# Optimization experiments

Measured on AMD Instinct MI355X. Metric: run time of the kernel, lower is better.

The kernel has to match this reference:

```python
import jax, jax.numpy as jnp
import numpy as np

N_GROUPS = 8
TOPK_GROUPS = 4
TOPK = 8
ROUTE_SCALE = 2.5


def setup_inputs() -> dict:
    key = jax.random.key(0)
    k1, k2, k3 = jax.random.split(key, 3)
    T, D, E = 8192, 7168, 256
    x = jax.random.normal(k1, (T, D), dtype=jnp.float32)
    weight = jax.random.normal(k2, (E, D), dtype=jnp.float32) * 0.02
    bias = jax.random.normal(k3, (E,), dtype=jnp.float32) * 0.02
    return {"x": x, "weight": weight, "bias": bias}


def reference(x, weight, bias):
    T = x.shape[0]
    # gate linear + sigmoid scores (score_func == 'sigmoid', computed in fp32)
    logits = jnp.einsum("td,ed->te", x, weight)  # [T, E]
    scores = jax.nn.sigmoid(logits.astype(jnp.float32))
    origin_scores = scores
    s = scores + bias  # bias present since dim == 7168
    # grouped scores: [T, G, E/G]
    sg = s.reshape(T, N_GROUPS, -1)
    # bias branch: group score = sum of top-2 per group
    top2, _ = jax.lax.top_k(sg, 2)
    group_scores = top2.sum(axis=-1)  # [T, G]
    # keep top `topk_groups` groups, zero out the rest
    _, gidx = jax.lax.top_k(group_scores, TOPK_GROUPS)  # [T, topk_groups]
    mask = jax.nn.one_hot(gidx, N_GROUPS, dtype=sg.dtype).sum(axis=1)  # [T, G]
    s_masked = (sg * mask[:, :, None]).reshape(T, -1)  # [T, E]
    # per-token expert top-k on masked scores
    _, expert_indices = jax.lax.top_k(s_masked, TOPK)  # [T, topk]
    # gather unbiased scores, normalize (sigmoid branch), scale
    weights = jnp.take_along_axis(origin_scores, expert_indices, axis=-1)
    weights = weights / weights.sum(axis=-1, keepdims=True)
    weights = weights * ROUTE_SCALE
    return weights.astype(x.dtype), expert_indices
```

## Files before the change

kernel.cpp:

```cpp
#include <hip/hip_runtime.h>
#include <cmath>

#define TT 8192
#define NE 256
#define ND 7168
#define NGRP 8
#define TOPKG 4
#define TOPK 8
#define ROUTE_SCALE 2.5f

#define NKT (ND / 32)
#define NNT (NE / 16)

#define TM 64
#define XPITCH 40

typedef _Float16 half8_ __attribute__((ext_vector_type(8)));
typedef _Float16 half4_ __attribute__((ext_vector_type(4)));
typedef float float4_ __attribute__((ext_vector_type(4)));

__global__ __launch_bounds__(256) void conv_w_kernel(
    const float* __restrict__ w, _Float16* __restrict__ whF,
    _Float16* __restrict__ wlF)
{
    const int gid  = blockIdx.x * 256 + threadIdx.x;
    const int lane = gid & 63;
    const int pair = gid >> 6;
    const int kt   = pair % NKT;
    const int nt   = pair / NKT;
    const int n  = nt * 16 + (lane & 15);
    const int kb = kt * 32 + (lane >> 4) * 8;
    const float* src = w + (size_t)n * ND + kb;
    const float4 v0 = *reinterpret_cast<const float4*>(src);
    const float4 v1 = *reinterpret_cast<const float4*>(src + 4);
    const float vs[8] = {v0.x, v0.y, v0.z, v0.w, v1.x, v1.y, v1.z, v1.w};
    half8_ h, l;
    #pragma unroll
    for (int j = 0; j < 8; ++j) {
        const _Float16 hi = (_Float16)vs[j];
        h[j] = hi;
        l[j] = (_Float16)(vs[j] - (float)hi);
    }
    const size_t off = ((size_t)pair * 64 + lane) * 8;
    *reinterpret_cast<half8_*>(whF + off) = h;
    *reinterpret_cast<half8_*>(wlF + off) = l;
}

__global__ __launch_bounds__(256, 2) void gemm_kernel(
    const float* __restrict__ x, const _Float16* __restrict__ whF,
    const _Float16* __restrict__ wlF, float* __restrict__ partial,
    int K_slice)
{
    __shared__ _Float16 Xh[TM][XPITCH];
    __shared__ _Float16 Xl[TM][XPITCH];

    const int tid  = threadIdx.x;
    const int lane = tid & 63;
    const int nq   = tid >> 6;
    const int t0   = blockIdx.x * TM;
    const int ks   = blockIdx.y;
    const int kbeg = ks * K_slice;
    const int kt0  = kbeg >> 5;
    const int nchunks = K_slice >> 5;

    const int q  = lane >> 4;
    const int cn = lane & 15;

    float4_ acc[4][4];
    #pragma unroll
    for (int i = 0; i < 4; ++i)
        #pragma unroll
        for (int j = 0; j < 4; ++j) acc[i][j] = (float4_)0.0f;

    const int srow0 = tid >> 3;
    const int sc4   = tid & 7;

    for (int c = 0; c < nchunks; ++c) {
        const int k0 = kbeg + c * 32;
        #pragma unroll
        for (int i = 0; i < 2; ++i) {
            const int row = srow0 + i * 32;
            const float4 v = *reinterpret_cast<const float4*>(
                x + (size_t)(t0 + row) * ND + k0 + sc4 * 4);
            const float vs[4] = {v.x, v.y, v.z, v.w};
            half4_ h, l;
            #pragma unroll
            for (int j = 0; j < 4; ++j) {
                const _Float16 hi = (_Float16)vs[j];
                h[j] = hi;
                l[j] = (_Float16)(vs[j] - (float)hi);
            }
            *reinterpret_cast<half4_*>(&Xh[row][sc4 * 4]) = h;
            *reinterpret_cast<half4_*>(&Xl[row][sc4 * 4]) = l;
        }
        __syncthreads();

        half8_ ah[4], al[4];
        #pragma unroll
        for (int mt = 0; mt < 4; ++mt) {
            ah[mt] = *reinterpret_cast<const half8_*>(&Xh[mt * 16 + cn][q * 8]);
            al[mt] = *reinterpret_cast<const half8_*>(&Xl[mt * 16 + cn][q * 8]);
        }
        const int kt = kt0 + c;
        half8_ bh[4], bl[4];
        #pragma unroll
        for (int ntl = 0; ntl < 4; ++ntl) {
            const size_t off =
                ((size_t)((nq * 4 + ntl) * NKT + kt) * 64 + lane) * 8;
            bh[ntl] = *reinterpret_cast<const half8_*>(whF + off);
            bl[ntl] = *reinterpret_cast<const half8_*>(wlF + off);
        }
        #pragma unroll
        for (int mt = 0; mt < 4; ++mt)
            #pragma unroll
            for (int ntl = 0; ntl < 4; ++ntl) {
                acc[mt][ntl] = __builtin_amdgcn_mfma_f32_16x16x32_f16(
                    ah[mt], bh[ntl], acc[mt][ntl], 0, 0, 0);
                acc[mt][ntl] = __builtin_amdgcn_mfma_f32_16x16x32_f16(
                    al[mt], bh[ntl], acc[mt][ntl], 0, 0, 0);
                acc[mt][ntl] = __builtin_amdgcn_mfma_f32_16x16x32_f16(
                    ah[mt], bl[ntl], acc[mt][ntl], 0, 0, 0);
            }
        __syncthreads();
    }

    #pragma unroll
    for (int mt = 0; mt < 4; ++mt)
        #pragma unroll
        for (int r = 0; r < 4; ++r) {
            const int t = t0 + mt * 16 + q * 4 + r;
            float* rowp = partial + ((size_t)ks * TT + t) * NE;
            #pragma unroll
            for (int ntl = 0; ntl < 4; ++ntl)
                rowp[nq * 64 + ntl * 16 + cn] = acc[mt][ntl][r];
        }
}

__global__ __launch_bounds__(256) void routing_kernel(
    const float* __restrict__ partial, const float* __restrict__ bias,
    float* __restrict__ out_w, float* __restrict__ out_i, int kslices)
{
    const int lane = threadIdx.x & 63;
    const int t = blockIdx.x * 4 + (threadIdx.x >> 6);

    float4 a = make_float4(0.f, 0.f, 0.f, 0.f);
    for (int s = 0; s < kslices; ++s) {
        const float4 p = *reinterpret_cast<const float4*>(
            partial + ((size_t)s * TT + t) * NE + lane * 4);
        a.x += p.x; a.y += p.y; a.z += p.z; a.w += p.w;
    }
    const float4 b4 = *reinterpret_cast<const float4*>(bias + lane * 4);
    const float lg[4] = {a.x, a.y, a.z, a.w};
    const float bs[4] = {b4.x, b4.y, b4.z, b4.w};
    float sg[4], sv[4];
    #pragma unroll
    for (int j = 0; j < 4; ++j) {
        sg[j] = 1.0f / (1.0f + expf(-lg[j]));
        sv[j] = sg[j] + bs[j];
    }

    float m1 = -1e30f, m2 = -1e30f;
    #pragma unroll
    for (int j = 0; j < 4; ++j) {
        if (sv[j] > m1)      { m2 = m1; m1 = sv[j]; }
        else if (sv[j] > m2) { m2 = sv[j]; }
    }
    #pragma unroll
    for (int off = 1; off <= 4; off <<= 1) {
        const float o1 = __shfl_xor(m1, off, 64);
        const float o2 = __shfl_xor(m2, off, 64);
        if (o1 > m1) { m2 = fmaxf(m1, o2); m1 = o1; }
        else         { m2 = fmaxf(m2, o1); }
    }
    const float gs = m1 + m2;

    float gv[NGRP];
    #pragma unroll
    for (int g = 0; g < NGRP; ++g) gv[g] = __shfl(gs, g * 8, 64);
    unsigned keep = 0;
    #pragma unroll
    for (int r = 0; r < TOPKG; ++r) {
        int best = 0; float bvv = -1e30f;
        #pragma unroll
        for (int g = 0; g < NGRP; ++g) {
            const bool taken = (keep >> g) & 1u;
            if (!taken && gv[g] > bvv) { bvv = gv[g]; best = g; }
        }
        keep |= 1u << best;
    }

    const bool kept = (keep >> (lane >> 3)) & 1u;
    float rv[4];
    #pragma unroll
    for (int j = 0; j < 4; ++j) rv[j] = kept ? sv[j] : 0.0f;

    float wsum = 0.f, myw = 0.f;
    int myi = 0;
    #pragma unroll
    for (int r = 0; r < TOPK; ++r) {
        float bv = -1e30f, bo = 0.f; int bi = 0x7fffffff;
        #pragma unroll
        for (int j = 0; j < 4; ++j)
            if (rv[j] > bv) { bv = rv[j]; bi = lane * 4 + j; bo = sg[j]; }
        #pragma unroll
        for (int off = 1; off < 64; off <<= 1) {
            const float ov = __shfl_xor(bv, off, 64);
            const int   oi = __shfl_xor(bi, off, 64);
            const float oo = __shfl_xor(bo, off, 64);
            if (ov > bv || (ov == bv && oi < bi)) { bv = ov; bi = oi; bo = oo; }
        }
        if ((bi >> 2) == lane) rv[bi & 3] = -1e30f;
        wsum += bo;
        if (lane == r) { myw = bo; myi = bi; }
    }
    const float scale = ROUTE_SCALE / wsum;
    if (lane < TOPK) {
        out_w[(size_t)t * TOPK + lane] = myw * scale;
        out_i[(size_t)t * TOPK + lane] = (float)myi;
    }
}

extern "C" void kernel_launch(void* const* d_in, const int* in_sizes, int n_in,
                              void* d_out, int out_size, void* d_ws, size_t ws_size,
                              hipStream_t stream) {
    const float* x    = (const float*)d_in[0];
    const float* w    = (const float*)d_in[1];
    const float* bias = (const float*)d_in[2];

    float* out_w = (float*)d_out;
    float* out_i = (float*)d_out + (size_t)TT * TOPK;

    const size_t wfrag_bytes = (size_t)NE * ND * sizeof(_Float16);
    _Float16* whF = (_Float16*)d_ws;
    _Float16* wlF = (_Float16*)((char*)d_ws + wfrag_bytes);
    float* partial = (float*)((char*)d_ws + 2 * wfrag_bytes);

    const size_t part1 = (size_t)TT * NE * sizeof(float);
    int kslices = 1;
    if (ws_size >= 2 * wfrag_bytes + 4 * part1) kslices = 4;
    else if (ws_size >= 2 * wfrag_bytes + 2 * part1) kslices = 2;
    const int K_slice = ND / kslices;

    conv_w_kernel<<<(NNT * NKT * 64) / 256, 256, 0, stream>>>(w, whF, wlF);

    dim3 ggrid(TT / TM, kslices);
    gemm_kernel<<<ggrid, 256, 0, stream>>>(x, whF, wlF, partial, K_slice);

    routing_kernel<<<TT / 4, 256, 0, stream>>>(partial, bias, out_w, out_i, kslices);
}
```

Before: 415.4 us.

## Double-buffer X tiles and prefetch weight fragments in gemm; allow 8 K-slices

The gemm main loop becomes software-pipelined. X tiles go into double-buffered shared memory, and the x and B-fragment global loads for the next chunks are issued before the current MFMAs, so there is one barrier per chunk instead of two. When the workspace is large enough the K dimension is also split into 8 slices instead of 4, which launches more blocks. The costs are higher register pressure from the prefetched fragments and more partial-sum traffic in the routing kernel.

Measured after the change: 390.9 us. 5.9% less time.

```diff
diff --git a/kernel.cpp b/kernel.cpp
--- a/kernel.cpp
+++ b/kernel.cpp
@@ -14,6 +14,7 @@
 
 #define TM 64
 #define XPITCH 40
+#define BSTRN ((size_t)NKT * 512)
 
 typedef _Float16 half8_ __attribute__((ext_vector_type(8)));
 typedef _Float16 half4_ __attribute__((ext_vector_type(4)));
@@ -51,8 +52,8 @@
     const _Float16* __restrict__ wlF, float* __restrict__ partial,
     int K_slice)
 {
-    __shared__ _Float16 Xh[TM][XPITCH];
-    __shared__ _Float16 Xl[TM][XPITCH];
+    __shared__ _Float16 XhL[2][TM * XPITCH];
+    __shared__ _Float16 XlL[2][TM * XPITCH];
 
     const int tid  = threadIdx.x;
     const int lane = tid & 63;
@@ -65,64 +66,106 @@
 
     const int q  = lane >> 4;
     const int cn = lane & 15;
-
-    float4_ acc[4][4];
-    #pragma unroll
-    for (int i = 0; i < 4; ++i)
-        #pragma unroll
-        for (int j = 0; j < 4; ++j) acc[i][j] = (float4_)0.0f;
-
     const int srow0 = tid >> 3;
     const int sc4   = tid & 7;
 
-    for (int c = 0; c < nchunks; ++c) {
-        const int k0 = kbeg + c * 32;
-        #pragma unroll
-        for (int i = 0; i < 2; ++i) {
-            const int row = srow0 + i * 32;
-            const float4 v = *reinterpret_cast<const float4*>(
-                x + (size_t)(t0 + row) * ND + k0 + sc4 * 4);
-            const float vs[4] = {v.x, v.y, v.z, v.w};
-            half4_ h, l;
-            #pragma unroll
-            for (int j = 0; j < 4; ++j) {
-                const _Float16 hi = (_Float16)vs[j];
-                h[j] = hi;
-                l[j] = (_Float16)(vs[j] - (float)hi);
-            }
-            *reinterpret_cast<half4_*>(&Xh[row][sc4 * 4]) = h;
-            *reinterpret_cast<half4_*>(&Xl[row][sc4 * 4]) = l;
-        }
-        __syncthreads();
-
-        half8_ ah[4], al[4];
-        #pragma unroll
-        for (int mt = 0; mt < 4; ++mt) {
-            ah[mt] = *reinterpret_cast<const half8_*>(&Xh[mt * 16 + cn][q * 8]);
-            al[mt] = *reinterpret_cast<const half8_*>(&Xl[mt * 16 + cn][q * 8]);
-        }
-        const int kt = kt0 + c;
-        half8_ bh[4], bl[4];
-        #pragma unroll
-        for (int ntl = 0; ntl < 4; ++ntl) {
-            const size_t off =
-                ((size_t)((nq * 4 + ntl) * NKT + kt) * 64 + lane) * 8;
-            bh[ntl] = *reinterpret_cast<const half8_*>(whF + off);
-            bl[ntl] = *reinterpret_cast<const half8_*>(wlF + off);
-        }
-        #pragma unroll
-        for (int mt = 0; mt < 4; ++mt)
-            #pragma unroll
-            for (int ntl = 0; ntl < 4; ++ntl) {
-                acc[mt][ntl] = __builtin_amdgcn_mfma_f32_16x16x32_f16(
-                    ah[mt], bh[ntl], acc[mt][ntl], 0, 0, 0);
-                acc[mt][ntl] = __builtin_amdgcn_mfma_f32_16x16x32_f16(
-                    al[mt], bh[ntl], acc[mt][ntl], 0, 0, 0);
-                acc[mt][ntl] = __builtin_amdgcn_mfma_f32_16x16x32_f16(
-                    ah[mt], bl[ntl], acc[mt][ntl], 0, 0, 0);
-            }
-        __syncthreads();
-    }
+    float4_ acc[4][4];
+    #pragma unroll
+    for (int i = 0; i < 4; ++i)
+        #pragma unroll
+        for (int j = 0; j < 4; ++j) acc[i][j] = (float4_)0.0f;
+
+    const float* xp0 = x + (size_t)(t0 + srow0) * ND + kbeg + sc4 * 4;
+    const float* xp1 = xp0 + (size_t)32 * ND;
+    const _Float16* bh0 = whF + (size_t)(nq * 4) * BSTRN + (size_t)kt0 * 512 + lane * 8;
+    const _Float16* bl0 = wlF + (size_t)(nq * 4) * BSTRN + (size_t)kt0 * 512 + lane * 8;
+
+    float4 xv[2][2];
+    half8_ Bf[2][8];
+
+    xv[0][0] = *reinterpret_cast<const float4*>(xp0);
+    xv[0][1] = *reinterpret_cast<const float4*>(xp1);
+    xv[1][0] = *reinterpret_cast<const float4*>(xp0 + 32);
+    xv[1][1] = *reinterpret_cast<const float4*>(xp1 + 32);
+    #pragma unroll
+    for (int ntl = 0; ntl < 4; ++ntl) {
+        Bf[0][ntl * 2 + 0] = *reinterpret_cast<const half8_*>(bh0 + (size_t)ntl * BSTRN);
+        Bf[0][ntl * 2 + 1] = *reinterpret_cast<const half8_*>(bl0 + (size_t)ntl * BSTRN);
+    }
+    #pragma unroll
+    for (int i = 0; i < 2; ++i) {
+        const float4 v = xv[0][i];
+        const float vs[4] = {v.x, v.y, v.z, v.w};
+        half4_ h, l;
+        #pragma unroll
+        for (int j = 0; j < 4; ++j) {
+            const _Float16 hi = (_Float16)vs[j];
+            h[j] = hi; l[j] = (_Float16)(vs[j] - (float)hi);
+        }
+        const int soff = (srow0 + i * 32) * XPITCH + sc4 * 4;
+        *reinterpret_cast<half4_*>(&XhL[0][soff]) = h;
+        *reinterpret_cast<half4_*>(&XlL[0][soff]) = l;
+    }
+    __syncthreads();
+
+#define STEP(P, C)                                                           \
+    {                                                                        \
+        if ((C) + 2 < nchunks) {  \
+            xv[P][0] = *reinterpret_cast<const float4*>(xp0 + ((C) + 2) * 32); \
+            xv[P][1] = *reinterpret_cast<const float4*>(xp1 + ((C) + 2) * 32); \
+        }                                                                    \
+        if ((C) + 1 < nchunks) {                     \
+            _Pragma("unroll")                                                \
+            for (int ntl = 0; ntl < 4; ++ntl) {                              \
+                Bf[(P) ^ 1][ntl * 2 + 0] = *reinterpret_cast<const half8_*>( \
+                    bh0 + (size_t)ntl * BSTRN + ((C) + 1) * 512);            \
+                Bf[(P) ^ 1][ntl * 2 + 1] = *reinterpret_cast<const half8_*>( \
+                    bl0 + (size_t)ntl * BSTRN + ((C) + 1) * 512);            \
+            }                                                                \
+        }                                                                    \
+        half8_ ah[4], al[4];                                                 \
+        _Pragma("unroll")                                                    \
+        for (int mt = 0; mt < 4; ++mt) {                                     \
+            ah[mt] = *reinterpret_cast<const half8_*>(                       \
+                &XhL[P][(mt * 16 + cn) * XPITCH + q * 8]);                   \
+            al[mt] = *reinterpret_cast<const half8_*>(                       \
+                &XlL[P][(mt * 16 + cn) * XPITCH + q * 8]);                   \
+        }                                                                    \
+        _Pragma("unroll")                                                    \
+        for (int mt = 0; mt < 4; ++mt)                                       \
+            _Pragma("unroll")                                                \
+            for (int ntl = 0; ntl < 4; ++ntl) {                              \
+                acc[mt][ntl] = __builtin_amdgcn_mfma_f32_16x16x32_f16(       \
+                    ah[mt], Bf[P][ntl * 2 + 0], acc[mt][ntl], 0, 0, 0);      \
+                acc[mt][ntl] = __builtin_amdgcn_mfma_f32_16x16x32_f16(       \
+                    al[mt], Bf[P][ntl * 2 + 0], acc[mt][ntl], 0, 0, 0);      \
+                acc[mt][ntl] = __builtin_amdgcn_mfma_f32_16x16x32_f16(       \
+                    ah[mt], Bf[P][ntl * 2 + 1], acc[mt][ntl], 0, 0, 0);      \
+            }                                                                \
+        if ((C) + 1 < nchunks) {  \
+            _Pragma("unroll")                                                \
+            for (int i = 0; i < 2; ++i) {                                    \
+                const float4 v = xv[(P) ^ 1][i];                             \
+                const float vs[4] = {v.x, v.y, v.z, v.w};                    \
+                half4_ h, l;                                                 \
+                _Pragma("unroll")                                            \
+                for (int j = 0; j < 4; ++j) {                                \
+                    const _Float16 hi = (_Float16)vs[j];                     \
+                    h[j] = hi; l[j] = (_Float16)(vs[j] - (float)hi);         \
+                }                                                            \
+                const int soff = (srow0 + i * 32) * XPITCH + sc4 * 4;        \
+                *reinterpret_cast<half4_*>(&XhL[(P) ^ 1][soff]) = h;         \
+                *reinterpret_cast<half4_*>(&XlL[(P) ^ 1][soff]) = l;         \
+            }                                                                \
+        }                                                                    \
+        __syncthreads();                                                     \
+    }
+
+    for (int c = 0; c < nchunks; c += 2) {
+        STEP(0, c)
+        STEP(1, c + 1)
+    }
+#undef STEP
 
     #pragma unroll
     for (int mt = 0; mt < 4; ++mt)
@@ -237,7 +280,8 @@
 
     const size_t part1 = (size_t)TT * NE * sizeof(float);
     int kslices = 1;
-    if (ws_size >= 2 * wfrag_bytes + 4 * part1) kslices = 4;
+    if      (ws_size >= 2 * wfrag_bytes + 8 * part1) kslices = 8;
+    else if (ws_size >= 2 * wfrag_bytes + 4 * part1) kslices = 4;
     else if (ws_size >= 2 * wfrag_bytes + 2 * part1) kslices = 2;
     const int K_slice = ND / kslices;
 
```

## Load X fragments directly into registers with double-buffered prefetch, drop LDS staging

Applied to the files above, without the earlier changes.

The GEMM kernel stops staging X through shared memory. Each wave now loads its X fragments straight from global memory into registers and splits them into fp16 hi/lo parts there. X and B fragments are double-buffered in registers so the next chunk's loads overlap the current MFMAs, and both __syncthreads per chunk go away. MFMAs are regrouped by pass, and the K split can go up to 8 slices when workspace allows. The trade-off is that every one of the four waves now loads and converts the same X tile redundantly, register pressure rises, and a larger partial buffer must be reduced.

New measurement: 501.4 us. 1.21x slower.

```diff
diff --git a/kernel.cpp b/kernel.cpp
--- a/kernel.cpp
+++ b/kernel.cpp
@@ -11,12 +11,10 @@
 
 #define NKT (ND / 32)
 #define NNT (NE / 16)
-
 #define TM 64
-#define XPITCH 40
+#define BSTRN ((size_t)NKT * 512)
 
 typedef _Float16 half8_ __attribute__((ext_vector_type(8)));
-typedef _Float16 half4_ __attribute__((ext_vector_type(4)));
 typedef float float4_ __attribute__((ext_vector_type(4)));
 
 __global__ __launch_bounds__(256) void conv_w_kernel(
@@ -51,9 +49,6 @@
     const _Float16* __restrict__ wlF, float* __restrict__ partial,
     int K_slice)
 {
-    __shared__ _Float16 Xh[TM][XPITCH];
-    __shared__ _Float16 Xl[TM][XPITCH];
-
     const int tid  = threadIdx.x;
     const int lane = tid & 63;
     const int nq   = tid >> 6;
@@ -72,57 +67,89 @@
         #pragma unroll
         for (int j = 0; j < 4; ++j) acc[i][j] = (float4_)0.0f;
 
-    const int srow0 = tid >> 3;
-    const int sc4   = tid & 7;
-
-    for (int c = 0; c < nchunks; ++c) {
-        const int k0 = kbeg + c * 32;
-        #pragma unroll
-        for (int i = 0; i < 2; ++i) {
-            const int row = srow0 + i * 32;
-            const float4 v = *reinterpret_cast<const float4*>(
-                x + (size_t)(t0 + row) * ND + k0 + sc4 * 4);
-            const float vs[4] = {v.x, v.y, v.z, v.w};
-            half4_ h, l;
-            #pragma unroll
-            for (int j = 0; j < 4; ++j) {
-                const _Float16 hi = (_Float16)vs[j];
-                h[j] = hi;
-                l[j] = (_Float16)(vs[j] - (float)hi);
-            }
-            *reinterpret_cast<half4_*>(&Xh[row][sc4 * 4]) = h;
-            *reinterpret_cast<half4_*>(&Xl[row][sc4 * 4]) = l;
-        }
-        __syncthreads();
-
-        half8_ ah[4], al[4];
-        #pragma unroll
-        for (int mt = 0; mt < 4; ++mt) {
-            ah[mt] = *reinterpret_cast<const half8_*>(&Xh[mt * 16 + cn][q * 8]);
-            al[mt] = *reinterpret_cast<const half8_*>(&Xl[mt * 16 + cn][q * 8]);
-        }
-        const int kt = kt0 + c;
-        half8_ bh[4], bl[4];
-        #pragma unroll
-        for (int ntl = 0; ntl < 4; ++ntl) {
-            const size_t off =
-                ((size_t)((nq * 4 + ntl) * NKT + kt) * 64 + lane) * 8;
-            bh[ntl] = *reinterpret_cast<const half8_*>(whF + off);
-            bl[ntl] = *reinterpret_cast<const half8_*>(wlF + off);
-        }
-        #pragma unroll
-        for (int mt = 0; mt < 4; ++mt)
-            #pragma unroll
-            for (int ntl = 0; ntl < 4; ++ntl) {
-                acc[mt][ntl] = __builtin_amdgcn_mfma_f32_16x16x32_f16(
-                    ah[mt], bh[ntl], acc[mt][ntl], 0, 0, 0);
-                acc[mt][ntl] = __builtin_amdgcn_mfma_f32_16x16x32_f16(
-                    al[mt], bh[ntl], acc[mt][ntl], 0, 0, 0);
-                acc[mt][ntl] = __builtin_amdgcn_mfma_f32_16x16x32_f16(
-                    ah[mt], bl[ntl], acc[mt][ntl], 0, 0, 0);
-            }
-        __syncthreads();
-    }
+    const float* xl = x + (size_t)(t0 + cn) * ND + kbeg + q * 8;
+    const _Float16* bh0 = whF + (size_t)(nq * 4) * BSTRN + (size_t)kt0 * 512 + lane * 8;
+    const _Float16* bl0 = wlF + (size_t)(nq * 4) * BSTRN + (size_t)kt0 * 512 + lane * 8;
+
+    float4 xv[2][4][2];
+    half8_ Bf[2][8];
+
+    #pragma unroll
+    for (int mt = 0; mt < 4; ++mt) {
+        const float* p = xl + (size_t)(mt * 16) * ND;
+        xv[0][mt][0] = *reinterpret_cast<const float4*>(p);
+        xv[0][mt][1] = *reinterpret_cast<const float4*>(p + 4);
+        xv[1][mt][0] = *reinterpret_cast<const float4*>(p + 32);
+        xv[1][mt][1] = *reinterpret_cast<const float4*>(p + 36);
+    }
+    #pragma unroll
+    for (int ntl = 0; ntl < 4; ++ntl) {
+        Bf[0][ntl * 2 + 0] = *reinterpret_cast<const half8_*>(bh0 + (size_t)ntl * BSTRN);
+        Bf[0][ntl * 2 + 1] = *reinterpret_cast<const half8_*>(bl0 + (size_t)ntl * BSTRN);
+    }
+
+#define STEP(P, C)                                                             \
+    {                                                                          \
+                          \
+        half8_ ah[4], al[4];                                                   \
+        _Pragma("unroll")                                                      \
+        for (int mt = 0; mt < 4; ++mt) {                                       \
+            const float4 v0 = xv[P][mt][0];                                    \
+            const float4 v1 = xv[P][mt][1];                                    \
+            const float vs[8] = {v0.x, v0.y, v0.z, v0.w,                       \
+                                 v1.x, v1.y, v1.z, v1.w};                      \
+            _Pragma("unroll")                                                  \
+            for (int j = 0; j < 8; ++j) {                                      \
+                const _Float16 hi = (_Float16)vs[j];                           \
+                ah[mt][j] = hi;                                                \
+                al[mt][j] = (_Float16)(vs[j] - (float)hi);                     \
+            }                                                                  \
+        }                                                                      \
+                \
+        if ((C) + 2 < nchunks) {                                               \
+            _Pragma("unroll")                                                  \
+            for (int mt = 0; mt < 4; ++mt) {                                   \
+                const float* p = xl + (size_t)(mt * 16) * ND + ((C) + 2) * 32; \
+                xv[P][mt][0] = *reinterpret_cast<const float4*>(p);            \
+                xv[P][mt][1] = *reinterpret_cast<const float4*>(p + 4);        \
+            }                                                                  \
+        }                                                                      \
+                                              \
+        if ((C) + 1 < nchunks) {                                               \
+            _Pragma("unroll")                                                  \
+            for (int ntl = 0; ntl < 4; ++ntl) {                                \
+                Bf[(P) ^ 1][ntl * 2 + 0] = *reinterpret_cast<const half8_*>(   \
+                    bh0 + (size_t)ntl * BSTRN + ((C) + 1) * 512);              \
+                Bf[(P) ^ 1][ntl * 2 + 1] = *reinterpret_cast<const half8_*>(   \
+                    bl0 + (size_t)ntl * BSTRN + ((C) + 1) * 512);              \
+            }                                                                  \
+        }                                                                      \
+            \
+        _Pragma("unroll")                                                      \
+        for (int mt = 0; mt < 4; ++mt)                                         \
+            _Pragma("unroll")                                                  \
+            for (int ntl = 0; ntl < 4; ++ntl)                                  \
+                acc[mt][ntl] = __builtin_amdgcn_mfma_f32_16x16x32_f16(         \
+                    ah[mt], Bf[P][ntl * 2 + 0], acc[mt][ntl], 0, 0, 0);        \
+        _Pragma("unroll")                                                      \
+        for (int mt = 0; mt < 4; ++mt)                                         \
+            _Pragma("unroll")                                                  \
+            for (int ntl = 0; ntl < 4; ++ntl)                                  \
+                acc[mt][ntl] = __builtin_amdgcn_mfma_f32_16x16x32_f16(         \
+                    al[mt], Bf[P][ntl * 2 + 0], acc[mt][ntl], 0, 0, 0);        \
+        _Pragma("unroll")                                                      \
+        for (int mt = 0; mt < 4; ++mt)                                         \
+            _Pragma("unroll")                                                  \
+            for (int ntl = 0; ntl < 4; ++ntl)                                  \
+                acc[mt][ntl] = __builtin_amdgcn_mfma_f32_16x16x32_f16(         \
+                    ah[mt], Bf[P][ntl * 2 + 1], acc[mt][ntl], 0, 0, 0);        \
+    }
+
+    for (int c = 0; c < nchunks; c += 2) {
+        STEP(0, c)
+        STEP(1, c + 1)
+    }
+#undef STEP
 
     #pragma unroll
     for (int mt = 0; mt < 4; ++mt)
@@ -237,7 +264,8 @@
 
     const size_t part1 = (size_t)TT * NE * sizeof(float);
     int kslices = 1;
-    if (ws_size >= 2 * wfrag_bytes + 4 * part1) kslices = 4;
+    if      (ws_size >= 2 * wfrag_bytes + 8 * part1) kslices = 8;
+    else if (ws_size >= 2 * wfrag_bytes + 4 * part1) kslices = 4;
     else if (ws_size >= 2 * wfrag_bytes + 2 * part1) kslices = 2;
     const int K_slice = ND / kslices;
 
```
